# Kernel tuning notes

Measured on AMD Instinct MI355X. Metric: run time of the kernel, lower is better.

## Reference

```python
import jax, jax.numpy as jnp
import numpy as np

N_NODES = 32
GAT_OUT = 64
LSTM_H = 128
N_CLS = 4
NEG_SLOPE = 0.2


def setup_inputs() -> dict:
    key = jax.random.key(0)
    ks = jax.random.split(key, 12)
    B, T, E = 32, 512, 96
    F, H = GAT_OUT, LSTM_H
    s = 0.05
    return {
        "x_seq": jax.random.normal(ks[0], (B, T, N_NODES), jnp.float32),
        "edge_index": jax.random.randint(ks[1], (2, E), 0, N_NODES, jnp.int32),
        # GATConv params (heads=1): lin weight [in=1, F], attention vectors [F], bias [F]
        "w_gat": jax.random.normal(ks[2], (1, F), jnp.float32) * s,
        "att_src": jax.random.normal(ks[3], (F,), jnp.float32) * s,
        "att_dst": jax.random.normal(ks[4], (F,), jnp.float32) * s,
        "b_gat": jnp.zeros((F,), jnp.float32),
        # LSTM params, torch gate order (i, f, g, o)
        "W_ih": jax.random.normal(ks[5], (N_NODES * F, 4 * H), jnp.float32) * s,
        "W_hh": jax.random.normal(ks[6], (H, 4 * H), jnp.float32) * s,
        "b_ih": jnp.zeros((4 * H,), jnp.float32),
        "b_hh": jnp.zeros((4 * H,), jnp.float32),
        # classifier
        "W_fc": jax.random.normal(ks[7], (H, N_CLS), jnp.float32) * s,
        "b_fc": jnp.zeros((N_CLS,), jnp.float32),
    }


def _forward(x_seq, edge_index, w_gat, att_src, att_dst, b_gat,
             W_ih, W_hh, b_ih, b_hh, W_fc, b_fc):
    B, T, N = x_seq.shape
    F = w_gat.shape[1]
    H = W_hh.shape[0]

    # --- GAT over all (B,T) steps at once (PyG GATConv, heads=1, self-loops) ---
    loops = jnp.arange(N, dtype=edge_index.dtype)
    src = jnp.concatenate([edge_index[0], loops])  # [Et]
    dst = jnp.concatenate([edge_index[1], loops])  # [Et]
    Et = src.shape[0]

    h = x_seq[..., None] * w_gat            # [B,T,N,F] (in_channels=1 linear)
    a_s = h @ att_src                        # [B,T,N]
    a_d = h @ att_dst                        # [B,T,N]
    e = a_s[..., src] + a_d[..., dst]        # [B,T,Et]
    e = jnp.where(e > 0, e, NEG_SLOPE * e)   # LeakyReLU(0.2)

    # segment softmax over destination node, batched over B*T
    e2 = jnp.moveaxis(e, -1, 0).reshape(Et, B * T)
    m = jax.ops.segment_max(e2, dst, num_segments=N)        # [N,B*T]
    ex = jnp.exp(e2 - m[dst])
    z = jax.ops.segment_sum(ex, dst, num_segments=N)        # [N,B*T]
    alpha = ex / z[dst]                                      # [Et,B*T]
    alpha = jnp.moveaxis(alpha.reshape(Et, B, T), 0, -1)     # [B,T,Et]

    msg = alpha[..., None] * h[:, :, src, :]                 # [B,T,Et,F]
    onehot = (dst[:, None] == jnp.arange(N)).astype(h.dtype)  # [Et,N]
    out = jnp.einsum('btef,en->btnf', msg, onehot) + b_gat    # [B,T,N,F]

    seq = out.reshape(B, T, N * F)           # [B,T,2048]

    # --- single-layer LSTM (batch_first), torch gate order i,f,g,o ---
    xw = seq @ W_ih + (b_ih + b_hh)          # [B,T,4H]

    def step(carry, xw_t):
        hs, cs = carry
        g = xw_t + hs @ W_hh                 # [B,4H]
        i, f, gg, o = jnp.split(g, 4, axis=-1)
        cs = jax.nn.sigmoid(f) * cs + jax.nn.sigmoid(i) * jnp.tanh(gg)
        hs = jax.nn.sigmoid(o) * jnp.tanh(cs)
        return (hs, cs), None

    h0 = jnp.zeros((B, H), seq.dtype)
    (h_last, _), _ = jax.lax.scan(step, (h0, h0), jnp.moveaxis(xw, 1, 0))

    return h_last @ W_fc + b_fc              # [B,num_classes]


def reference(x_seq, edge_index, w_gat, att_src, att_dst, b_gat,
              W_ih, W_hh, b_ih, b_hh, W_fc, b_fc):
    return _forward(x_seq, edge_index, w_gat, att_src, att_dst, b_gat,
                    W_ih, W_hh, b_ih, b_hh, W_fc, b_fc)
```

## Files before the change

kernel.cpp:

```cpp
#include <hip/hip_runtime.h>

#define NN 32
#define FF 64
#define HH 128
#define G4 512
#define BB 32
#define TT 512
#define ET 128
#define NPOS (BB*TT)

__device__ __forceinline__ float frcp(float x) { return __builtin_amdgcn_rcpf(x); }

__global__ __launch_bounds__(512) void prep_kernel(const float* __restrict__ w_gat,
                                                   const float* __restrict__ b_gat,
                                                   const float* __restrict__ W_ih,
                                                   float* __restrict__ W_eff,
                                                   float* __restrict__ biasp) {
  int j = threadIdx.x;
  int n = blockIdx.x;
  float accw = 0.f, accb = 0.f;
#pragma unroll 8
  for (int f = 0; f < FF; ++f) {
    float wv = W_ih[(n * FF + f) * G4 + j];
    accw = fmaf(w_gat[f], wv, accw);
    accb = fmaf(b_gat[f], wv, accb);
  }
  W_eff[n * G4 + j] = accw;
  biasp[n * G4 + j] = accb;
}

__global__ __launch_bounds__(512) void prep2_kernel(const float* __restrict__ biasp,
                                                    const float* __restrict__ b_ih,
                                                    const float* __restrict__ b_hh,
                                                    const float* __restrict__ w_gat,
                                                    const float* __restrict__ att_src,
                                                    const float* __restrict__ att_dst,
                                                    const int* __restrict__ ei,
                                                    float* __restrict__ bias_eff,
                                                    float* __restrict__ scal,
                                                    int* __restrict__ srt_g,
                                                    int* __restrict__ off_g) {
  __shared__ int cnt[NN];
  __shared__ int off[NN + 1];
  __shared__ int srt[ET];
  int j = threadIdx.x;
  if (j < NN) cnt[j] = 0;
  float acc = b_ih[j] + b_hh[j];
#pragma unroll
  for (int n = 0; n < NN; ++n) acc += biasp[n * G4 + j];
  bias_eff[j] = acc;
  if (j == 0) {
    float cs = 0.f, cd = 0.f;
    for (int f = 0; f < FF; ++f) {
      cs = fmaf(w_gat[f], att_src[f], cs);
      cd = fmaf(w_gat[f], att_dst[f], cd);
    }
    scal[0] = cs;
    scal[1] = cd;
  }
  __syncthreads();
  int s = 0, d = 0, tk = 0;
  if (j < ET) {
    if (j < 96) { s = ei[j]; d = ei[96 + j]; }
    else { s = j - 96; d = j - 96; }
    tk = atomicAdd(&cnt[d], 1);
  }
  __syncthreads();
  if (j == 0) {
    off[0] = 0;
    for (int n = 0; n < NN; ++n) off[n + 1] = off[n] + cnt[n];
  }
  __syncthreads();
  if (j < ET) srt[off[d] + tk] = s;
  __syncthreads();
  if (j < ET) srt_g[j] = srt[j];
  if (j < NN + 1) off_g[j] = off[j];
}

__global__ __launch_bounds__(128) void prep3_kernel(const float* __restrict__ W_hh,
                                                    float* __restrict__ Wt) {
  int tid = blockIdx.x;
  int m = threadIdx.x;
  int r = tid >> 2, kq = tid & 3;
  int g = m >> 5, kk = m & 31;
  Wt[tid * 128 + m] = W_hh[(kq * 32 + kk) * G4 + g * 128 + r];
}

__global__ __launch_bounds__(256) void gatxw_kernel(const float* __restrict__ x_seq,
                                                    const int* __restrict__ srt_g,
                                                    const int* __restrict__ off_g,
                                                    const float* __restrict__ scal,
                                                    const float* __restrict__ W_eff,
                                                    const float* __restrict__ bias_eff,
                                                    float* __restrict__ xw) {
  __shared__ int srt[ET];
  __shared__ int offs[NN + 1];
  __shared__ float xs[8 * 32];
  __shared__ float sl[8 * 32];
  int tid = threadIdx.x;
  int posbase = blockIdx.x * 8;
  float we0[NN], we1[NN];
#pragma unroll
  for (int nn = 0; nn < NN; ++nn) {
    we0[nn] = W_eff[nn * G4 + tid];
    we1[nn] = W_eff[nn * G4 + 256 + tid];
  }
  float b0 = bias_eff[tid], b1 = bias_eff[256 + tid];
  if (tid < ET) srt[tid] = srt_g[tid];
  if (tid < NN + 1) offs[tid] = off_g[tid];
  int p = tid >> 5, n = tid & 31;
  xs[tid] = x_seq[posbase * NN + tid];
  __syncthreads();
  float cs = scal[0], cd = scal[1];
  int base = p * 32;
  int e0 = offs[n], e1 = offs[n + 1];
  float xn = xs[base + n];
  float cdxn = cd * xn;
  float m = -3.0e38f;
  for (int e = e0; e < e1; ++e) {
    float ev = fmaf(cs, xs[base + srt[e]], cdxn);
    ev = ev > 0.f ? ev : 0.2f * ev;
    m = fmaxf(m, ev);
  }
  float z = 0.f, sa = 0.f;
  for (int e = e0; e < e1; ++e) {
    float xsv = xs[base + srt[e]];
    float ev = fmaf(cs, xsv, cdxn);
    ev = ev > 0.f ? ev : 0.2f * ev;
    float ex = __expf(ev - m);
    z += ex;
    sa = fmaf(ex, xsv, sa);
  }
  sl[p * 32 + n] = sa * frcp(z);
  __syncthreads();
  for (int pp = 0; pp < 8; ++pp) {
    const float4* sp = (const float4*)&sl[pp * 32];
    float a0 = b0, a1 = b1;
#pragma unroll
    for (int q = 0; q < 8; ++q) {
      float4 sv = sp[q];
      a0 = fmaf(sv.x, we0[4 * q], a0);
      a0 = fmaf(sv.y, we0[4 * q + 1], a0);
      a0 = fmaf(sv.z, we0[4 * q + 2], a0);
      a0 = fmaf(sv.w, we0[4 * q + 3], a0);
      a1 = fmaf(sv.x, we1[4 * q], a1);
      a1 = fmaf(sv.y, we1[4 * q + 1], a1);
      a1 = fmaf(sv.z, we1[4 * q + 2], a1);
      a1 = fmaf(sv.w, we1[4 * q + 3], a1);
    }
    size_t row = (size_t)(posbase + pp) * G4;
    xw[row + tid] = a0;
    xw[row + 256 + tid] = a1;
  }
}


#define PK16(HP, W0, W1, W2, W3, SRC2A, SRC2B, SRC2C, SRC2D) \
  "v_pk_fma_f32 v[216:217], v[" HP "], v[" W0 "], " SRC2A "\n\t" \
  "v_pk_fma_f32 v[218:219], v[" HP "], v[" W1 "], " SRC2B "\n\t" \
  "v_pk_fma_f32 v[220:221], v[" HP "], v[" W2 "], " SRC2C "\n\t" \
  "v_pk_fma_f32 v[222:223], v[" HP "], v[" W3 "], " SRC2D "\n\t"

#define PK_BLOCK \
  PK16("32:33", "64:65",  "96:97",   "128:129", "160:161", "0", "0", "0", "0") \
  PK16("34:35", "66:67",  "98:99",   "130:131", "162:163", "v[216:217]", "v[218:219]", "v[220:221]", "v[222:223]") \
  PK16("36:37", "68:69",  "100:101", "132:133", "164:165", "v[216:217]", "v[218:219]", "v[220:221]", "v[222:223]") \
  PK16("38:39", "70:71",  "102:103", "134:135", "166:167", "v[216:217]", "v[218:219]", "v[220:221]", "v[222:223]") \
  PK16("40:41", "72:73",  "104:105", "136:137", "168:169", "v[216:217]", "v[218:219]", "v[220:221]", "v[222:223]") \
  PK16("42:43", "74:75",  "106:107", "138:139", "170:171", "v[216:217]", "v[218:219]", "v[220:221]", "v[222:223]") \
  PK16("44:45", "76:77",  "108:109", "140:141", "172:173", "v[216:217]", "v[218:219]", "v[220:221]", "v[222:223]") \
  PK16("46:47", "78:79",  "110:111", "142:143", "174:175", "v[216:217]", "v[218:219]", "v[220:221]", "v[222:223]") \
  PK16("48:49", "80:81",  "112:113", "144:145", "176:177", "v[216:217]", "v[218:219]", "v[220:221]", "v[222:223]") \
  PK16("50:51", "82:83",  "114:115", "146:147", "178:179", "v[216:217]", "v[218:219]", "v[220:221]", "v[222:223]") \
  PK16("52:53", "84:85",  "116:117", "148:149", "180:181", "v[216:217]", "v[218:219]", "v[220:221]", "v[222:223]") \
  PK16("54:55", "86:87",  "118:119", "150:151", "182:183", "v[216:217]", "v[218:219]", "v[220:221]", "v[222:223]") \
  PK16("56:57", "88:89",  "120:121", "152:153", "184:185", "v[216:217]", "v[218:219]", "v[220:221]", "v[222:223]") \
  PK16("58:59", "90:91",  "122:123", "154:155", "186:187", "v[216:217]", "v[218:219]", "v[220:221]", "v[222:223]") \
  PK16("60:61", "92:93",  "124:125", "156:157", "188:189", "v[216:217]", "v[218:219]", "v[220:221]", "v[222:223]") \
  PK16("62:63", "94:95",  "126:127", "158:159", "190:191", "v[216:217]", "v[218:219]", "v[220:221]", "v[222:223]")

#define PHASE(XLOAD, XUSE, RD, WR) \
  "global_load_dword " XLOAD ", v194, %[xwb]\n\t" \
  "v_add_u32 v194, 0x800, v194\n\t" \
  "ds_read_b128 v[32:35], " RD "\n\t" \
  "ds_read_b128 v[36:39], " RD " offset:16\n\t" \
  "ds_read_b128 v[40:43], " RD " offset:32\n\t" \
  "ds_read_b128 v[44:47], " RD " offset:48\n\t" \
  "ds_read_b128 v[48:51], " RD " offset:64\n\t" \
  "ds_read_b128 v[52:55], " RD " offset:80\n\t" \
  "ds_read_b128 v[56:59], " RD " offset:96\n\t" \
  "ds_read_b128 v[60:63], " RD " offset:112\n\t" \
  "s_waitcnt lgkmcnt(0)\n\t" \
  PK_BLOCK \
  "v_add_f32 v204, v216, v217\n\t" \
  "v_add_f32 v205, v218, v219\n\t" \
  "v_add_f32 v206, v220, v221\n\t" \
  "v_add_f32 v207, v222, v223\n\t" \
  "s_waitcnt vmcnt(1)\n\t" \
  "v_fmac_f32 v204, " XUSE ", v200\n\t" \
  "v_fmac_f32 v205, " XUSE ", v201\n\t" \
  "v_fmac_f32 v206, " XUSE ", v202\n\t" \
  "v_fmac_f32 v207, " XUSE ", v203\n\t" \
  "v_add_f32_dpp v204, v204, v204 quad_perm:[1,0,3,2] row_mask:0xf bank_mask:0xf\n\t" \
  "v_add_f32_dpp v205, v205, v205 quad_perm:[1,0,3,2] row_mask:0xf bank_mask:0xf\n\t" \
  "v_add_f32_dpp v206, v206, v206 quad_perm:[1,0,3,2] row_mask:0xf bank_mask:0xf\n\t" \
  "v_add_f32_dpp v207, v207, v207 quad_perm:[1,0,3,2] row_mask:0xf bank_mask:0xf\n\t" \
  "v_add_f32_dpp v204, v204, v204 quad_perm:[2,3,0,1] row_mask:0xf bank_mask:0xf\n\t" \
  "v_add_f32_dpp v205, v205, v205 quad_perm:[2,3,0,1] row_mask:0xf bank_mask:0xf\n\t" \
  "v_add_f32_dpp v206, v206, v206 quad_perm:[2,3,0,1] row_mask:0xf bank_mask:0xf\n\t" \
  "v_add_f32_dpp v207, v207, v207 quad_perm:[2,3,0,1] row_mask:0xf bank_mask:0xf\n\t" \
  "v_mul_f32 v208, 0xbfb8aa3b, v204\n\t" \
  "v_mul_f32 v209, 0xbfb8aa3b, v205\n\t" \
  "v_mul_f32 v210, 0x4038aa3b, v206\n\t" \
  "v_mul_f32 v211, 0xbfb8aa3b, v207\n\t" \
  "v_exp_f32 v208, v208\n\t" \
  "v_exp_f32 v209, v209\n\t" \
  "v_exp_f32 v210, v210\n\t" \
  "v_exp_f32 v211, v211\n\t" \
  "v_add_f32 v208, 1.0, v208\n\t" \
  "v_add_f32 v209, 1.0, v209\n\t" \
  "v_add_f32 v210, 1.0, v210\n\t" \
  "v_add_f32 v211, 1.0, v211\n\t" \
  "v_rcp_f32 v208, v208\n\t" \
  "v_rcp_f32 v209, v209\n\t" \
  "v_rcp_f32 v210, v210\n\t" \
  "v_rcp_f32 v211, v211\n\t" \
  "v_fma_f32 v210, -2.0, v210, 1.0\n\t" \
  "v_mul_f32 v212, v208, v210\n\t" \
  "v_fma_f32 v199, v209, v199, v212\n\t" \
  "v_mul_f32 v214, 0x4038aa3b, v199\n\t" \
  "v_exp_f32 v214, v214\n\t" \
  "s_nop 1\n\t" \
  "v_add_f32 v214, 1.0, v214\n\t" \
  "v_rcp_f32 v214, v214\n\t" \
  "s_nop 1\n\t" \
  "v_fma_f32 v214, -2.0, v214, 1.0\n\t" \
  "v_mul_f32 v213, v211, v214\n\t" \
  "ds_write_b32 " WR ", v213\n\t" \
  "s_waitcnt lgkmcnt(0)\n\t" \
  "s_barrier\n\t"

__global__ __launch_bounds__(512, 2) void lstm_kernel(const float* __restrict__ xw,
                                                      const float* __restrict__ Wt,
                                                      const float* __restrict__ W_fc,
                                                      const float* __restrict__ b_fc,
                                                      float* __restrict__ out) {
  __shared__ __align__(16) float lds[320];
  int b = blockIdx.x, tid = threadIdx.x;
  int r = tid >> 2, kq = tid & 3;
  if (tid < 320) lds[tid] = 0.f;
  const float* xwb = xw + (size_t)b * TT * G4;
  float xv0 = xwb[kq * 128 + r];
  unsigned xoff0 = (unsigned)((kq * 128 + r + G4) * 4);
  unsigned wtoff = (unsigned)(tid * 512);
  unsigned lbase = (unsigned)(uintptr_t)&lds[0];
  unsigned rda = lbase + kq * 160;
  unsigned rdb = rda + 640;
  unsigned wra = lbase + (((r >> 5) * 40 + (r & 31)) << 2);
  unsigned wrb = wra + 640;
  float mh0 = (kq == 0) ? 1.f : 0.f;
  float mh1 = (kq == 1) ? 1.f : 0.f;
  float mh2 = (kq == 2) ? 1.f : 0.f;
  float mh3 = (kq == 3) ? 1.f : 0.f;
  __syncthreads();
  asm volatile(
    "v_mov_b32 v194, %[xo]\n\t"
    "v_mov_b32 v193, %[xv0]\n\t"
    "v_mov_b32 v195, %[rda]\n\t"
    "v_mov_b32 v196, %[rdb]\n\t"
    "v_mov_b32 v197, %[wra]\n\t"
    "v_mov_b32 v198, %[wrb]\n\t"
    "v_mov_b32 v199, 0\n\t"
    "v_mov_b32 v200, %[m0]\n\t"
    "v_mov_b32 v201, %[m1]\n\t"
    "v_mov_b32 v202, %[m2]\n\t"
    "v_mov_b32 v203, %[m3]\n\t"
    "global_load_dwordx4 v[64:67], %[wto], %[wtb] offset:0\n\t"
    "global_load_dwordx4 v[68:71], %[wto], %[wtb] offset:16\n\t"
    "global_load_dwordx4 v[72:75], %[wto], %[wtb] offset:32\n\t"
    "global_load_dwordx4 v[76:79], %[wto], %[wtb] offset:48\n\t"
    "global_load_dwordx4 v[80:83], %[wto], %[wtb] offset:64\n\t"
    "global_load_dwordx4 v[84:87], %[wto], %[wtb] offset:80\n\t"
    "global_load_dwordx4 v[88:91], %[wto], %[wtb] offset:96\n\t"
    "global_load_dwordx4 v[92:95], %[wto], %[wtb] offset:112\n\t"
    "global_load_dwordx4 v[96:99], %[wto], %[wtb] offset:128\n\t"
    "global_load_dwordx4 v[100:103], %[wto], %[wtb] offset:144\n\t"
    "global_load_dwordx4 v[104:107], %[wto], %[wtb] offset:160\n\t"
    "global_load_dwordx4 v[108:111], %[wto], %[wtb] offset:176\n\t"
    "global_load_dwordx4 v[112:115], %[wto], %[wtb] offset:192\n\t"
    "global_load_dwordx4 v[116:119], %[wto], %[wtb] offset:208\n\t"
    "global_load_dwordx4 v[120:123], %[wto], %[wtb] offset:224\n\t"
    "global_load_dwordx4 v[124:127], %[wto], %[wtb] offset:240\n\t"
    "global_load_dwordx4 v[128:131], %[wto], %[wtb] offset:256\n\t"
    "global_load_dwordx4 v[132:135], %[wto], %[wtb] offset:272\n\t"
    "global_load_dwordx4 v[136:139], %[wto], %[wtb] offset:288\n\t"
    "global_load_dwordx4 v[140:143], %[wto], %[wtb] offset:304\n\t"
    "global_load_dwordx4 v[144:147], %[wto], %[wtb] offset:320\n\t"
    "global_load_dwordx4 v[148:151], %[wto], %[wtb] offset:336\n\t"
    "global_load_dwordx4 v[152:155], %[wto], %[wtb] offset:352\n\t"
    "global_load_dwordx4 v[156:159], %[wto], %[wtb] offset:368\n\t"
    "global_load_dwordx4 v[160:163], %[wto], %[wtb] offset:384\n\t"
    "global_load_dwordx4 v[164:167], %[wto], %[wtb] offset:400\n\t"
    "global_load_dwordx4 v[168:171], %[wto], %[wtb] offset:416\n\t"
    "global_load_dwordx4 v[172:175], %[wto], %[wtb] offset:432\n\t"
    "global_load_dwordx4 v[176:179], %[wto], %[wtb] offset:448\n\t"
    "global_load_dwordx4 v[180:183], %[wto], %[wtb] offset:464\n\t"
    "global_load_dwordx4 v[184:187], %[wto], %[wtb] offset:480\n\t"
    "global_load_dwordx4 v[188:191], %[wto], %[wtb] offset:496\n\t"
    "s_waitcnt vmcnt(0)\n\t"
    "s_movk_i32 s20, 0x100\n\t"
    "L_lstm_%=:\n\t"
    PHASE("v192", "v193", "v195", "v198")
    PHASE("v193", "v192", "v196", "v197")
    "s_sub_u32 s20, s20, 1\n\t"
    "s_cmp_lg_u32 s20, 0\n\t"
    "s_cbranch_scc1 L_lstm_%=\n\t"
    "s_waitcnt vmcnt(0) lgkmcnt(0)\n\t"
    :
    : [xwb]"s"(xwb), [wtb]"s"(Wt), [wto]"v"(wtoff), [xo]"v"(xoff0), [xv0]"v"(xv0),
      [rda]"v"(rda), [rdb]"v"(rdb), [wra]"v"(wra), [wrb]"v"(wrb),
      [m0]"v"(mh0), [m1]"v"(mh1), [m2]"v"(mh2), [m3]"v"(mh3)
    : "memory", "scc", "s20",
      "v32","v33","v34","v35","v36","v37","v38","v39",
      "v40","v41","v42","v43","v44","v45","v46","v47",
      "v48","v49","v50","v51","v52","v53","v54","v55",
      "v56","v57","v58","v59","v60","v61","v62","v63",
      "v64","v65","v66","v67","v68","v69","v70","v71",
      "v72","v73","v74","v75","v76","v77","v78","v79",
      "v80","v81","v82","v83","v84","v85","v86","v87",
      "v88","v89","v90","v91","v92","v93","v94","v95",
      "v96","v97","v98","v99","v100","v101","v102","v103",
      "v104","v105","v106","v107","v108","v109","v110","v111",
      "v112","v113","v114","v115","v116","v117","v118","v119",
      "v120","v121","v122","v123","v124","v125","v126","v127",
      "v128","v129","v130","v131","v132","v133","v134","v135",
      "v136","v137","v138","v139","v140","v141","v142","v143",
      "v144","v145","v146","v147","v148","v149","v150","v151",
      "v152","v153","v154","v155","v156","v157","v158","v159",
      "v160","v161","v162","v163","v164","v165","v166","v167",
      "v168","v169","v170","v171","v172","v173","v174","v175",
      "v176","v177","v178","v179","v180","v181","v182","v183",
      "v184","v185","v186","v187","v188","v189","v190","v191",
      "v192","v193","v194","v195","v196","v197","v198","v199",
      "v200","v201","v202","v203","v204","v205","v206","v207",
      "v208","v209","v210","v211","v212","v213","v214","v215",
      "v216","v217","v218","v219","v220","v221","v222","v223");
  __syncthreads();
  if (tid < 4) {
    float acc = b_fc[tid];
#pragma unroll 8
    for (int k = 0; k < HH; ++k)
      acc = fmaf(lds[(k >> 5) * 40 + (k & 31)], W_fc[k * 4 + tid], acc);
    out[b * 4 + tid] = acc;
  }
}

extern "C" void kernel_launch(void* const* d_in, const int* in_sizes, int n_in,
                              void* d_out, int out_size, void* d_ws, size_t ws_size,
                              hipStream_t stream) {
  const float* x_seq   = (const float*)d_in[0];
  const int*   ei      = (const int*)d_in[1];
  const float* w_gat   = (const float*)d_in[2];
  const float* att_src = (const float*)d_in[3];
  const float* att_dst = (const float*)d_in[4];
  const float* b_gat   = (const float*)d_in[5];
  const float* W_ih    = (const float*)d_in[6];
  const float* W_hh    = (const float*)d_in[7];
  const float* b_ih    = (const float*)d_in[8];
  const float* b_hh    = (const float*)d_in[9];
  const float* W_fc    = (const float*)d_in[10];
  const float* b_fc    = (const float*)d_in[11];

  float* ws = (float*)d_ws;
  float* Wt       = ws;
  float* xw       = Wt + 65536;
  float* W_eff    = xw + (size_t)(NPOS + 1) * G4;
  float* bias_eff = W_eff + NN * G4;
  float* scal     = bias_eff + G4;
  float* biasp    = scal + 2;
  int*   srt_g    = (int*)(biasp + NN * G4);
  int*   off_g    = srt_g + ET;

  prep_kernel<<<NN, G4, 0, stream>>>(w_gat, b_gat, W_ih, W_eff, biasp);
  prep2_kernel<<<1, G4, 0, stream>>>(biasp, b_ih, b_hh, w_gat, att_src, att_dst, ei,
                                     bias_eff, scal, srt_g, off_g);
  prep3_kernel<<<G4, 128, 0, stream>>>(W_hh, Wt);
  gatxw_kernel<<<NPOS / 8, 256, 0, stream>>>(x_seq, srt_g, off_g, scal, W_eff, bias_eff, xw);
  lstm_kernel<<<BB, G4, 0, stream>>>(xw, Wt, W_fc, b_fc, (float*)d_out);
}
```

Measured before the change: 410.3 us.

## Deepen xw prefetch to four steps and split LDS waits per read

Inside the hand-written LSTM recurrence loop, the per-step xw input is now prefetched four timesteps ahead in a ring of four registers instead of one step ahead with two. The single lgkmcnt(0) wait before the packed-FMA block is also replaced by staggered waits, so FMAs start as soon as each ds_read lands. Both aim to hide global and LDS latency on the serial critical path of each step. The loop is unrolled four phases per iteration and the workspace padding grows to cover the extra over-read rows past the end.

```diff
diff --git a/kernel.cpp b/kernel.cpp
--- a/kernel.cpp
+++ b/kernel.cpp
@@ -155,33 +155,19 @@
 }
 
 
-#define PK16(HP, W0, W1, W2, W3, SRC2A, SRC2B, SRC2C, SRC2D) \
-  "v_pk_fma_f32 v[216:217], v[" HP "], v[" W0 "], " SRC2A "\n\t" \
-  "v_pk_fma_f32 v[218:219], v[" HP "], v[" W1 "], " SRC2B "\n\t" \
-  "v_pk_fma_f32 v[220:221], v[" HP "], v[" W2 "], " SRC2C "\n\t" \
-  "v_pk_fma_f32 v[222:223], v[" HP "], v[" W3 "], " SRC2D "\n\t"
-
-#define PK_BLOCK \
-  PK16("32:33", "64:65",  "96:97",   "128:129", "160:161", "0", "0", "0", "0") \
-  PK16("34:35", "66:67",  "98:99",   "130:131", "162:163", "v[216:217]", "v[218:219]", "v[220:221]", "v[222:223]") \
-  PK16("36:37", "68:69",  "100:101", "132:133", "164:165", "v[216:217]", "v[218:219]", "v[220:221]", "v[222:223]") \
-  PK16("38:39", "70:71",  "102:103", "134:135", "166:167", "v[216:217]", "v[218:219]", "v[220:221]", "v[222:223]") \
-  PK16("40:41", "72:73",  "104:105", "136:137", "168:169", "v[216:217]", "v[218:219]", "v[220:221]", "v[222:223]") \
-  PK16("42:43", "74:75",  "106:107", "138:139", "170:171", "v[216:217]", "v[218:219]", "v[220:221]", "v[222:223]") \
-  PK16("44:45", "76:77",  "108:109", "140:141", "172:173", "v[216:217]", "v[218:219]", "v[220:221]", "v[222:223]") \
-  PK16("46:47", "78:79",  "110:111", "142:143", "174:175", "v[216:217]", "v[218:219]", "v[220:221]", "v[222:223]") \
-  PK16("48:49", "80:81",  "112:113", "144:145", "176:177", "v[216:217]", "v[218:219]", "v[220:221]", "v[222:223]") \
-  PK16("50:51", "82:83",  "114:115", "146:147", "178:179", "v[216:217]", "v[218:219]", "v[220:221]", "v[222:223]") \
-  PK16("52:53", "84:85",  "116:117", "148:149", "180:181", "v[216:217]", "v[218:219]", "v[220:221]", "v[222:223]") \
-  PK16("54:55", "86:87",  "118:119", "150:151", "182:183", "v[216:217]", "v[218:219]", "v[220:221]", "v[222:223]") \
-  PK16("56:57", "88:89",  "120:121", "152:153", "184:185", "v[216:217]", "v[218:219]", "v[220:221]", "v[222:223]") \
-  PK16("58:59", "90:91",  "122:123", "154:155", "186:187", "v[216:217]", "v[218:219]", "v[220:221]", "v[222:223]") \
-  PK16("60:61", "92:93",  "124:125", "156:157", "188:189", "v[216:217]", "v[218:219]", "v[220:221]", "v[222:223]") \
-  PK16("62:63", "94:95",  "126:127", "158:159", "190:191", "v[216:217]", "v[218:219]", "v[220:221]", "v[222:223]")
-
-#define PHASE(XLOAD, XUSE, RD, WR) \
-  "global_load_dword " XLOAD ", v194, %[xwb]\n\t" \
-  "v_add_u32 v194, 0x800, v194\n\t" \
+#define PK16F(HP, W0, W1, W2, W3) \
+  "v_pk_fma_f32 v[216:217], v[" HP "], v[" W0 "], 0\n\t" \
+  "v_pk_fma_f32 v[218:219], v[" HP "], v[" W1 "], 0\n\t" \
+  "v_pk_fma_f32 v[220:221], v[" HP "], v[" W2 "], 0\n\t" \
+  "v_pk_fma_f32 v[222:223], v[" HP "], v[" W3 "], 0\n\t"
+
+#define PK16A(HP, W0, W1, W2, W3) \
+  "v_pk_fma_f32 v[216:217], v[" HP "], v[" W0 "], v[216:217]\n\t" \
+  "v_pk_fma_f32 v[218:219], v[" HP "], v[" W1 "], v[218:219]\n\t" \
+  "v_pk_fma_f32 v[220:221], v[" HP "], v[" W2 "], v[220:221]\n\t" \
+  "v_pk_fma_f32 v[222:223], v[" HP "], v[" W3 "], v[222:223]\n\t"
+
+#define PHASE(XSLOT, RD, WR) \
   "ds_read_b128 v[32:35], " RD "\n\t" \
   "ds_read_b128 v[36:39], " RD " offset:16\n\t" \
   "ds_read_b128 v[40:43], " RD " offset:32\n\t" \
@@ -190,17 +176,42 @@
   "ds_read_b128 v[52:55], " RD " offset:80\n\t" \
   "ds_read_b128 v[56:59], " RD " offset:96\n\t" \
   "ds_read_b128 v[60:63], " RD " offset:112\n\t" \
+  "s_waitcnt vmcnt(3)\n\t" \
+  "v_mov_b32 v215, " XSLOT "\n\t" \
+  "global_load_dword " XSLOT ", v194, %[xwb]\n\t" \
+  "v_add_u32 v194, 0x800, v194\n\t" \
+  "s_waitcnt lgkmcnt(7)\n\t" \
+  PK16F("32:33", "64:65",  "96:97",   "128:129", "160:161") \
+  PK16A("34:35", "66:67",  "98:99",   "130:131", "162:163") \
+  "s_waitcnt lgkmcnt(6)\n\t" \
+  PK16A("36:37", "68:69",  "100:101", "132:133", "164:165") \
+  PK16A("38:39", "70:71",  "102:103", "134:135", "166:167") \
+  "s_waitcnt lgkmcnt(5)\n\t" \
+  PK16A("40:41", "72:73",  "104:105", "136:137", "168:169") \
+  PK16A("42:43", "74:75",  "106:107", "138:139", "170:171") \
+  "s_waitcnt lgkmcnt(4)\n\t" \
+  PK16A("44:45", "76:77",  "108:109", "140:141", "172:173") \
+  PK16A("46:47", "78:79",  "110:111", "142:143", "174:175") \
+  "s_waitcnt lgkmcnt(3)\n\t" \
+  PK16A("48:49", "80:81",  "112:113", "144:145", "176:177") \
+  PK16A("50:51", "82:83",  "114:115", "146:147", "178:179") \
+  "s_waitcnt lgkmcnt(2)\n\t" \
+  PK16A("52:53", "84:85",  "116:117", "148:149", "180:181") \
+  PK16A("54:55", "86:87",  "118:119", "150:151", "182:183") \
+  "s_waitcnt lgkmcnt(1)\n\t" \
+  PK16A("56:57", "88:89",  "120:121", "152:153", "184:185") \
+  PK16A("58:59", "90:91",  "122:123", "154:155", "186:187") \
   "s_waitcnt lgkmcnt(0)\n\t" \
-  PK_BLOCK \
+  PK16A("60:61", "92:93",  "124:125", "156:157", "188:189") \
+  PK16A("62:63", "94:95",  "126:127", "158:159", "190:191") \
   "v_add_f32 v204, v216, v217\n\t" \
   "v_add_f32 v205, v218, v219\n\t" \
   "v_add_f32 v206, v220, v221\n\t" \
   "v_add_f32 v207, v222, v223\n\t" \
-  "s_waitcnt vmcnt(1)\n\t" \
-  "v_fmac_f32 v204, " XUSE ", v200\n\t" \
-  "v_fmac_f32 v205, " XUSE ", v201\n\t" \
-  "v_fmac_f32 v206, " XUSE ", v202\n\t" \
-  "v_fmac_f32 v207, " XUSE ", v203\n\t" \
+  "v_fmac_f32 v204, v215, v200\n\t" \
+  "v_fmac_f32 v205, v215, v201\n\t" \
+  "v_fmac_f32 v206, v215, v202\n\t" \
+  "v_fmac_f32 v207, v215, v203\n\t" \
   "v_add_f32_dpp v204, v204, v204 quad_perm:[1,0,3,2] row_mask:0xf bank_mask:0xf\n\t" \
   "v_add_f32_dpp v205, v205, v205 quad_perm:[1,0,3,2] row_mask:0xf bank_mask:0xf\n\t" \
   "v_add_f32_dpp v206, v206, v206 quad_perm:[1,0,3,2] row_mask:0xf bank_mask:0xf\n\t" \
@@ -250,8 +261,7 @@
   int r = tid >> 2, kq = tid & 3;
   if (tid < 320) lds[tid] = 0.f;
   const float* xwb = xw + (size_t)b * TT * G4;
-  float xv0 = xwb[kq * 128 + r];
-  unsigned xoff0 = (unsigned)((kq * 128 + r + G4) * 4);
+  unsigned xoff0 = (unsigned)((kq * 128 + r) * 4);
   unsigned wtoff = (unsigned)(tid * 512);
   unsigned lbase = (unsigned)(uintptr_t)&lds[0];
   unsigned rda = lbase + kq * 160;
@@ -265,7 +275,6 @@
   __syncthreads();
   asm volatile(
     "v_mov_b32 v194, %[xo]\n\t"
-    "v_mov_b32 v193, %[xv0]\n\t"
     "v_mov_b32 v195, %[rda]\n\t"
     "v_mov_b32 v196, %[rdb]\n\t"
     "v_mov_b32 v197, %[wra]\n\t"
@@ -275,6 +284,14 @@
     "v_mov_b32 v201, %[m1]\n\t"
     "v_mov_b32 v202, %[m2]\n\t"
     "v_mov_b32 v203, %[m3]\n\t"
+    "global_load_dword v224, v194, %[xwb]\n\t"
+    "v_add_u32 v194, 0x800, v194\n\t"
+    "global_load_dword v225, v194, %[xwb]\n\t"
+    "v_add_u32 v194, 0x800, v194\n\t"
+    "global_load_dword v226, v194, %[xwb]\n\t"
+    "v_add_u32 v194, 0x800, v194\n\t"
+    "global_load_dword v227, v194, %[xwb]\n\t"
+    "v_add_u32 v194, 0x800, v194\n\t"
     "global_load_dwordx4 v[64:67], %[wto], %[wtb] offset:0\n\t"
     "global_load_dwordx4 v[68:71], %[wto], %[wtb] offset:16\n\t"
     "global_load_dwordx4 v[72:75], %[wto], %[wtb] offset:32\n\t"
@@ -307,17 +324,19 @@
     "global_load_dwordx4 v[180:183], %[wto], %[wtb] offset:464\n\t"
     "global_load_dwordx4 v[184:187], %[wto], %[wtb] offset:480\n\t"
     "global_load_dwordx4 v[188:191], %[wto], %[wtb] offset:496\n\t"
-    "s_waitcnt vmcnt(0)\n\t"
-    "s_movk_i32 s20, 0x100\n\t"
+    "s_waitcnt vmcnt(4)\n\t"
+    "s_movk_i32 s20, 0x80\n\t"
     "L_lstm_%=:\n\t"
-    PHASE("v192", "v193", "v195", "v198")
-    PHASE("v193", "v192", "v196", "v197")
+    PHASE("v224", "v195", "v198")
+    PHASE("v225", "v196", "v197")
+    PHASE("v226", "v195", "v198")
+    PHASE("v227", "v196", "v197")
     "s_sub_u32 s20, s20, 1\n\t"
     "s_cmp_lg_u32 s20, 0\n\t"
     "s_cbranch_scc1 L_lstm_%=\n\t"
     "s_waitcnt vmcnt(0) lgkmcnt(0)\n\t"
     :
-    : [xwb]"s"(xwb), [wtb]"s"(Wt), [wto]"v"(wtoff), [xo]"v"(xoff0), [xv0]"v"(xv0),
+    : [xwb]"s"(xwb), [wtb]"s"(Wt), [wto]"v"(wtoff), [xo]"v"(xoff0),
       [rda]"v"(rda), [rdb]"v"(rdb), [wra]"v"(wra), [wrb]"v"(wrb),
       [m0]"v"(mh0), [m1]"v"(mh1), [m2]"v"(mh2), [m3]"v"(mh3)
     : "memory", "scc", "s20",
@@ -344,7 +363,8 @@
       "v192","v193","v194","v195","v196","v197","v198","v199",
       "v200","v201","v202","v203","v204","v205","v206","v207",
       "v208","v209","v210","v211","v212","v213","v214","v215",
-      "v216","v217","v218","v219","v220","v221","v222","v223");
+      "v216","v217","v218","v219","v220","v221","v222","v223",
+      "v224","v225","v226","v227");
   __syncthreads();
   if (tid < 4) {
     float acc = b_fc[tid];
@@ -374,7 +394,7 @@
   float* ws = (float*)d_ws;
   float* Wt       = ws;
   float* xw       = Wt + 65536;
-  float* W_eff    = xw + (size_t)(NPOS + 1) * G4;
+  float* W_eff    = xw + (size_t)(NPOS + 8) * G4;
   float* bias_eff = W_eff + NN * G4;
   float* scal     = bias_eff + G4;
   float* biasp    = scal + 2;
```

Measured after the change: 396.1 us. -3.5%, faster.
